# Performance work log

Measured on AMD Instinct MI355X. Metric: run time of the kernel, lower is better.

## Reference

```python
import jax, jax.numpy as jnp
import numpy as np

B, S, D, H = 2, 2048, 1024, 16
DK = D // H  # 64


def setup_inputs() -> dict:
    key = jax.random.key(0)
    ks = jax.random.split(key, 5)
    query_input = jax.random.normal(ks[0], (B, S, D), dtype=jnp.float32)
    # additive mask: 1.0 where attention is disallowed (causal upper triangle)
    mask = jnp.triu(jnp.ones((S, S), dtype=jnp.float32), k=1)[None, None, :, :]
    scale = 1.0 / np.sqrt(D)
    wq = jax.random.normal(ks[1], (D, D), dtype=jnp.float32) * scale
    wk = jax.random.normal(ks[2], (D, D), dtype=jnp.float32) * scale
    wv = jax.random.normal(ks[3], (D, D), dtype=jnp.float32) * scale
    wo = jax.random.normal(ks[4], (D, D), dtype=jnp.float32) * scale
    return {"query_input": query_input, "mask": mask, "wq": wq, "wk": wk, "wv": wv, "wo": wo}


def _split_heads(x):
    # [B, S, D] -> [B, H, S, DK]
    b, s, _ = x.shape
    return x.reshape(b, s, H, DK).transpose(0, 2, 1, 3)


def reference(query_input, mask, wq, wk, wv, wo):
    # self-attention: key_input = value_input = query_input
    q = _split_heads(query_input @ wq)  # [B, H, S, DK]
    k = _split_heads(query_input @ wk)
    v = _split_heads(query_input @ wv)
    scores = jnp.einsum('bhqd,bhkd->bhqk', q, k) / jnp.sqrt(jnp.float32(DK))
    scores = scores + mask * (-1e9)
    attn = jax.nn.softmax(scores, axis=-1)
    out = jnp.einsum('bhqk,bhkd->bhqd', attn, v)  # [B, H, S, DK]
    out = out.transpose(0, 2, 1, 3).reshape(query_input.shape[0], -1, D)
    return out @ wo
```

## Files before the change

kernel.cpp:

```cpp
#include <hip/hip_runtime.h>

typedef __attribute__((ext_vector_type(8))) short bf16x8;
typedef __attribute__((ext_vector_type(4))) float f32x4;
typedef __attribute__((ext_vector_type(4))) unsigned short u16x4;

#define S_LEN 2048
#define D_DIM 1024
#define NHEAD 16
#define DK 64
#define BH 32
#define MROWS 4096

__device__ __forceinline__ unsigned short f2bf(float f) {
    unsigned int u = __float_as_uint(f);
    u += 0x7fffu + ((u >> 16) & 1u);
    return (unsigned short)(u >> 16);
}

__device__ __forceinline__ unsigned int pk_bf16(float a, float b) {
    unsigned int r;
    asm("v_cvt_pk_bf16_f32 %0, %1, %2" : "=v"(r) : "v"(a), "v"(b));
    return r;
}

__device__ __forceinline__ float fexp2(float x) {
    return __builtin_amdgcn_exp2f(x);
}

__device__ __forceinline__ void gload16(const void* g, void* l) {
    __builtin_amdgcn_global_load_lds(
        (const __attribute__((address_space(1))) void*)g,
        (__attribute__((address_space(3))) void*)l, 16, 0, 0);
}

__global__ __launch_bounds__(256) void cast_x_kernel(const float* __restrict__ X,
                                                     unsigned short* __restrict__ Xb) {
    int idx = blockIdx.x * 256 + threadIdx.x;
    float4 v = ((const float4*)X)[idx];
    u16x4 o;
    o.x = f2bf(v.x); o.y = f2bf(v.y); o.z = f2bf(v.z); o.w = f2bf(v.w);
    ((u16x4*)Xb)[idx] = o;
}

__global__ __launch_bounds__(256) void wtrans_kernel(const float* __restrict__ wq,
                                                     const float* __restrict__ wk,
                                                     const float* __restrict__ wv,
                                                     const float* __restrict__ wo,
                                                     unsigned short* __restrict__ Wt) {
    int z = blockIdx.z;
    const float* W = (z == 0) ? wq : (z == 1) ? wk : (z == 2) ? wv : wo;
    unsigned short* O = Wt + (size_t)z * D_DIM * D_DIM;
    __shared__ float t[32][33];
    int tx = threadIdx.x, ty = threadIdx.y;
    int bx = blockIdx.x * 32;
    int by = blockIdx.y * 32;
#pragma unroll
    for (int i = 0; i < 4; ++i)
        t[ty + i * 8][tx] = W[(size_t)(by + ty + i * 8) * D_DIM + bx + tx];
    __syncthreads();
#pragma unroll
    for (int i = 0; i < 4; ++i)
        O[(size_t)(bx + ty + i * 8) * D_DIM + by + tx] = f2bf(t[tx][ty + i * 8]);
}

__device__ __forceinline__ void gemm_mainloop(const unsigned short* __restrict__ A,
                                              const unsigned short* __restrict__ Bt,
                                              int K, int m0, int n0,
                                              unsigned short* As, unsigned short* Bs,
                                              f32x4 acc[4][4]) {
    const int tid = threadIdx.x;
    const int lane = tid & 63, wid = tid >> 6;
    const int wr = wid >> 1, wc = wid & 1;
    const int fr = lane & 15, fk = (lane >> 4) * 8;
    for (int k0 = 0; k0 < K; k0 += 32) {
        __syncthreads();
#pragma unroll
        for (int c = 0; c < 2; ++c) {
            int idx = c * 256 + tid;
            int row = idx >> 2;
            int col = (idx & 3) * 8;
            int base = (c * 256 + wid * 64) * 8;
            gload16(&A[(size_t)(m0 + row) * K + k0 + col], &As[base]);
            gload16(&Bt[(size_t)(n0 + row) * K + k0 + col], &Bs[base]);
        }
        __syncthreads();
        bf16x8 af[4], bfr[4];
#pragma unroll
        for (int i = 0; i < 4; ++i)
            af[i] = *(const bf16x8*)&As[(wr * 64 + i * 16 + fr) * 32 + fk];
#pragma unroll
        for (int j = 0; j < 4; ++j)
            bfr[j] = *(const bf16x8*)&Bs[(wc * 64 + j * 16 + fr) * 32 + fk];
#pragma unroll
        for (int i = 0; i < 4; ++i)
#pragma unroll
            for (int j = 0; j < 4; ++j)
                acc[i][j] = __builtin_amdgcn_mfma_f32_16x16x32_bf16(af[i], bfr[j], acc[i][j], 0, 0, 0);
    }
}

#define QSCALE 0.18033688011112042f
__global__ __launch_bounds__(256) void gemm_qkv_kernel(const unsigned short* __restrict__ Xb,
                                                       const unsigned short* __restrict__ Wt,
                                                       unsigned short* __restrict__ QKV) {
    __shared__ __align__(16) unsigned short As[128 * 32];
    __shared__ __align__(16) unsigned short Bs[128 * 32];
    const unsigned short* Bt = Wt + (size_t)blockIdx.z * D_DIM * D_DIM;
    unsigned short* Out = QKV + (size_t)blockIdx.z * MROWS * D_DIM;
    int m0 = blockIdx.y * 128, n0 = blockIdx.x * 128;
    f32x4 acc[4][4] = {};
    gemm_mainloop(Xb, Bt, D_DIM, m0, n0, As, Bs, acc);
    const float qs = (blockIdx.z == 0) ? QSCALE : 1.0f;
    const int lane = threadIdx.x & 63, wid = threadIdx.x >> 6;
    const int wr = wid >> 1, wc = wid & 1;
#pragma unroll
    for (int i = 0; i < 4; ++i)
#pragma unroll
        for (int j = 0; j < 4; ++j)
#pragma unroll
            for (int r = 0; r < 4; ++r) {
                int gm = m0 + wr * 64 + i * 16 + (lane >> 4) * 4 + r;
                int gn = n0 + wc * 64 + j * 16 + (lane & 15);
                Out[(size_t)gm * D_DIM + gn] = f2bf(acc[i][j][r] * qs);
            }
}

__global__ __launch_bounds__(256) void vtrans_kernel(const unsigned short* __restrict__ V,
                                                     unsigned short* __restrict__ Vt) {
    __shared__ unsigned short tile[64][65];
    int bh = blockIdx.y;
    int b = bh >> 4, h = bh & 15;
    int s0 = blockIdx.x * 64;
    int t = threadIdx.x;
#pragma unroll
    for (int i = 0; i < 16; ++i) {
        int idx = i * 256 + t;
        int row = idx >> 6, col = idx & 63;
        tile[row][col] = V[((size_t)(b * S_LEN) + s0 + row) * D_DIM + h * DK + col];
    }
    __syncthreads();
#pragma unroll
    for (int i = 0; i < 16; ++i) {
        int idx = i * 256 + t;
        int dr = idx >> 6, sc = idx & 63;
        Vt[((size_t)bh * DK + dr) * S_LEN + s0 + sc] = tile[sc][dr];
    }
}

__global__ __launch_bounds__(512, 4) void attn_kernel(const unsigned short* __restrict__ QKV,
                                                      const unsigned short* __restrict__ Vt,
                                                      unsigned short* __restrict__ AO) {
    const int bh = blockIdx.x;
    const int y = blockIdx.y;
    const int qi = (y < 8) ? (15 - y) : (y - 8);
    const int tid = threadIdx.x, lane = tid & 63, wid = tid >> 6;
    const int fr = lane & 15, fkg = lane >> 4, fk = fkg * 8;
    const unsigned short* Q = QKV;
    const unsigned short* Kd = QKV + (size_t)MROWS * D_DIM;

    __shared__ __align__(16) unsigned short Ks[128][64];
    __shared__ __align__(16) unsigned short Vs[64][128];
    __shared__ __align__(16) unsigned short Ps[8][16][64];

    const int b = bh >> 4, h = bh & 15;
    const int rsw  = fr & 7;
    const int off0 = (fkg ^ rsw) * 8;
    const int off1 = ((4 + fkg) ^ rsw) * 8;

    const int i0 = tid, i1 = 512 + tid;
    const int kr0 = i0 >> 3, kc0 = ((i0 & 7) ^ (kr0 & 7)) * 8;
    const int kr1 = i1 >> 3, kc1 = ((i1 & 7) ^ (kr1 & 7)) * 8;
    const int vr0 = i0 >> 4, vc0 = ((i0 & 15) ^ (vr0 & 15)) * 8;
    const int vr1 = i1 >> 4, vc1 = ((i1 & 15) ^ (vr1 & 15)) * 8;
    const int sb0 = (wid * 64) * 8;
    const int sb1 = (512 + wid * 64) * 8;

    const int q0 = qi * 128;
    const int qr = q0 + wid * 16;

    bf16x8 qf0 = *(const bf16x8*)&Q[((size_t)(b * S_LEN) + qr + fr) * D_DIM + h * DK + fk];
    bf16x8 qf1 = *(const bf16x8*)&Q[((size_t)(b * S_LEN) + qr + fr) * D_DIM + h * DK + 32 + fk];

    f32x4 o[4] = {};
    float m = -1e30f, l = 0.f;
    const int ntiles = qi + 1;

    const unsigned short* kb = Kd + (size_t)(b * S_LEN) * D_DIM + h * DK;
    const unsigned short* vb = Vt + (size_t)bh * DK * S_LEN;

    gload16(kb + (size_t)kr0 * D_DIM + kc0, &Ks[0][0] + sb0);
    gload16(kb + (size_t)kr1 * D_DIM + kc1, &Ks[0][0] + sb1);
    gload16(vb + (size_t)vr0 * S_LEN + vc0, &Vs[0][0] + sb0);
    gload16(vb + (size_t)vr1 * S_LEN + vc1, &Vs[0][0] + sb1);

    for (int t = 0; t < ntiles; ++t) {
        __syncthreads();

        f32x4 s4[8];
        __builtin_amdgcn_s_setprio(1);
#pragma unroll
        for (int nj = 0; nj < 8; ++nj) {
            const unsigned short* krow = &Ks[nj * 16 + fr][0];
            bf16x8 kf0 = *(const bf16x8*)&krow[off0];
            bf16x8 kf1 = *(const bf16x8*)&krow[off1];
            f32x4 z = {};
            z = __builtin_amdgcn_mfma_f32_16x16x32_bf16(kf0, qf0, z, 0, 0, 0);
            z = __builtin_amdgcn_mfma_f32_16x16x32_bf16(kf1, qf1, z, 0, 0, 0);
            s4[nj] = z;
        }
        __builtin_amdgcn_s_setprio(0);

        if (t == ntiles - 1) {
            const int qoff = wid * 16 + fr;
#pragma unroll
            for (int nj = 0; nj < 8; ++nj)
#pragma unroll
                for (int r = 0; r < 4; ++r)
                    s4[nj][r] = (nj * 16 + fkg * 4 + r > qoff) ? -1e30f : s4[nj][r];
        }

        float mg[8];
#pragma unroll
        for (int nj = 0; nj < 8; ++nj)
            mg[nj] = fmaxf(fmaxf(s4[nj][0], s4[nj][1]), fmaxf(s4[nj][2], s4[nj][3]));
        float mt = fmaxf(fmaxf(fmaxf(mg[0], mg[1]), fmaxf(mg[2], mg[3])),
                         fmaxf(fmaxf(mg[4], mg[5]), fmaxf(mg[6], mg[7])));
        mt = fmaxf(mt, __shfl_xor(mt, 16, 64));
        mt = fmaxf(mt, __shfl_xor(mt, 32, 64));
        if (!__all(mt <= m + 8.0f)) {
            float mn = fmaxf(m, mt);
            float corr = fexp2(m - mn);
            m = mn;
            l *= corr;
            o[0] *= corr; o[1] *= corr; o[2] *= corr; o[3] *= corr;
        }
        float ps = 0.f;
        unsigned int pw[8][2];
#pragma unroll
        for (int nj = 0; nj < 8; ++nj) {
            float p0 = fexp2(s4[nj][0] - m);
            float p1 = fexp2(s4[nj][1] - m);
            float p2 = fexp2(s4[nj][2] - m);
            float p3 = fexp2(s4[nj][3] - m);
            ps += (p0 + p1) + (p2 + p3);
            pw[nj][0] = pk_bf16(p0, p1);
            pw[nj][1] = pk_bf16(p2, p3);
        }
        ps += __shfl_xor(ps, 16, 64);
        ps += __shfl_xor(ps, 32, 64);
        l += ps;

#pragma unroll
        for (int hf = 0; hf < 2; ++hf) {
#pragma unroll
            for (int nj = 0; nj < 4; ++nj) {
                int chunk = nj * 2 + (fkg >> 1);
                int el = (fkg & 1) * 4;
                *(uint2*)&Ps[wid][fr][((chunk ^ rsw) << 3) + el] =
                    make_uint2(pw[hf * 4 + nj][0], pw[hf * 4 + nj][1]);
            }
            bf16x8 pf0 = *(const bf16x8*)&Ps[wid][fr][off0];
            bf16x8 pf1 = *(const bf16x8*)&Ps[wid][fr][off1];
            __builtin_amdgcn_s_setprio(1);
#pragma unroll
            for (int j = 0; j < 4; ++j) {
                const unsigned short* vrow = &Vs[j * 16 + fr][0];
                bf16x8 vf0 = *(const bf16x8*)&vrow[((hf * 8 + fkg) ^ fr) * 8];
                bf16x8 vf1 = *(const bf16x8*)&vrow[((hf * 8 + 4 + fkg) ^ fr) * 8];
                o[j] = __builtin_amdgcn_mfma_f32_16x16x32_bf16(vf0, pf0, o[j], 0, 0, 0);
                o[j] = __builtin_amdgcn_mfma_f32_16x16x32_bf16(vf1, pf1, o[j], 0, 0, 0);
            }
            __builtin_amdgcn_s_setprio(0);
        }

        __syncthreads();
        if (t + 1 < ntiles) {
            const int kt = (t + 1) * 128;
            gload16(kb + (size_t)(kt + kr0) * D_DIM + kc0, &Ks[0][0] + sb0);
            gload16(kb + (size_t)(kt + kr1) * D_DIM + kc1, &Ks[0][0] + sb1);
            gload16(vb + (size_t)vr0 * S_LEN + kt + vc0, &Vs[0][0] + sb0);
            gload16(vb + (size_t)vr1 * S_LEN + kt + vc1, &Vs[0][0] + sb1);
        }
    }

    float inv = 1.0f / l;
    size_t rowoff = ((size_t)(b * S_LEN) + qr + fr) * D_DIM + h * DK;
#pragma unroll
    for (int j = 0; j < 4; ++j) {
        u16x4 w;
        w.x = f2bf(o[j][0] * inv); w.y = f2bf(o[j][1] * inv);
        w.z = f2bf(o[j][2] * inv); w.w = f2bf(o[j][3] * inv);
        *(u16x4*)&AO[rowoff + j * 16 + fkg * 4] = w;
    }
}

__global__ __launch_bounds__(256) void gemm_out_kernel(const unsigned short* __restrict__ AO,
                                                       const unsigned short* __restrict__ Wot,
                                                       float* __restrict__ out) {
    __shared__ __align__(16) unsigned short As[128 * 32];
    __shared__ __align__(16) unsigned short Bs[128 * 32];
    int m0 = blockIdx.y * 128, n0 = blockIdx.x * 128;
    f32x4 acc[4][4] = {};
    gemm_mainloop(AO, Wot, D_DIM, m0, n0, As, Bs, acc);
    const int lane = threadIdx.x & 63, wid = threadIdx.x >> 6;
    const int wr = wid >> 1, wc = wid & 1;
#pragma unroll
    for (int i = 0; i < 4; ++i)
#pragma unroll
        for (int j = 0; j < 4; ++j)
#pragma unroll
            for (int r = 0; r < 4; ++r) {
                int gm = m0 + wr * 64 + i * 16 + (lane >> 4) * 4 + r;
                int gn = n0 + wc * 64 + j * 16 + (lane & 15);
                out[(size_t)gm * D_DIM + gn] = acc[i][j][r];
            }
}

extern "C" void kernel_launch(void* const* d_in, const int* in_sizes, int n_in,
                              void* d_out, int out_size, void* d_ws, size_t ws_size,
                              hipStream_t stream) {
    (void)in_sizes; (void)n_in; (void)out_size; (void)ws_size;
    const float* X  = (const float*)d_in[0];
    const float* wq = (const float*)d_in[2];
    const float* wk = (const float*)d_in[3];
    const float* wv = (const float*)d_in[4];
    const float* wo = (const float*)d_in[5];

    char* ws = (char*)d_ws;
    unsigned short* Xb  = (unsigned short*)(ws);
    unsigned short* Wt  = (unsigned short*)(ws + ((size_t)8  << 20));
    unsigned short* QKV = (unsigned short*)(ws + ((size_t)16 << 20));
    unsigned short* Vt  = (unsigned short*)(ws + ((size_t)40 << 20));
    unsigned short* AO  = (unsigned short*)(ws + ((size_t)48 << 20));
    float* out = (float*)d_out;

    cast_x_kernel<<<4096, 256, 0, stream>>>(X, Xb);
    wtrans_kernel<<<dim3(32, 32, 4), dim3(32, 8), 0, stream>>>(wq, wk, wv, wo, Wt);
    gemm_qkv_kernel<<<dim3(8, 32, 3), 256, 0, stream>>>(Xb, Wt, QKV);
    vtrans_kernel<<<dim3(32, 32), 256, 0, stream>>>(QKV + (size_t)2 * MROWS * D_DIM, Vt);
    attn_kernel<<<dim3(32, 16), 512, 0, stream>>>(QKV, Vt, AO);
    gemm_out_kernel<<<dim3(8, 32), 256, 0, stream>>>(AO, Wt + (size_t)3 * D_DIM * D_DIM, out);
}
```

Before: 112.6 us.

## Pair light and heavy 64-row query tiles per attention block for causal balance

```diff
diff --git a/kernel.cpp b/kernel.cpp
--- a/kernel.cpp
+++ b/kernel.cpp
@@ -147,12 +147,11 @@
     }
 }
 
-__global__ __launch_bounds__(512, 4) void attn_kernel(const unsigned short* __restrict__ QKV,
+__global__ __launch_bounds__(256, 2) void attn_kernel(const unsigned short* __restrict__ QKV,
                                                       const unsigned short* __restrict__ Vt,
                                                       unsigned short* __restrict__ AO) {
     const int bh = blockIdx.x;
-    const int y = blockIdx.y;
-    const int qi = (y < 8) ? (15 - y) : (y - 8);
+    const int pair = blockIdx.y;
     const int tid = threadIdx.x, lane = tid & 63, wid = tid >> 6;
     const int fr = lane & 15, fkg = lane >> 4, fk = fkg * 8;
     const unsigned short* Q = QKV;
@@ -160,137 +159,144 @@
 
     __shared__ __align__(16) unsigned short Ks[128][64];
     __shared__ __align__(16) unsigned short Vs[64][128];
-    __shared__ __align__(16) unsigned short Ps[8][16][64];
+    __shared__ __align__(16) unsigned short Ps[4][16][64];
 
     const int b = bh >> 4, h = bh & 15;
     const int rsw  = fr & 7;
     const int off0 = (fkg ^ rsw) * 8;
     const int off1 = ((4 + fkg) ^ rsw) * 8;
 
-    const int i0 = tid, i1 = 512 + tid;
-    const int kr0 = i0 >> 3, kc0 = ((i0 & 7) ^ (kr0 & 7)) * 8;
-    const int kr1 = i1 >> 3, kc1 = ((i1 & 7) ^ (kr1 & 7)) * 8;
-    const int vr0 = i0 >> 4, vc0 = ((i0 & 15) ^ (vr0 & 15)) * 8;
-    const int vr1 = i1 >> 4, vc1 = ((i1 & 15) ^ (vr1 & 15)) * 8;
-    const int sb0 = (wid * 64) * 8;
-    const int sb1 = (512 + wid * 64) * 8;
-
-    const int q0 = qi * 128;
-    const int qr = q0 + wid * 16;
-
-    bf16x8 qf0 = *(const bf16x8*)&Q[((size_t)(b * S_LEN) + qr + fr) * D_DIM + h * DK + fk];
-    bf16x8 qf1 = *(const bf16x8*)&Q[((size_t)(b * S_LEN) + qr + fr) * D_DIM + h * DK + 32 + fk];
-
-    f32x4 o[4] = {};
-    float m = -1e30f, l = 0.f;
-    const int ntiles = qi + 1;
+    int kr[4], kc[4], vr[4], vc[4], sb[4];
+#pragma unroll
+    for (int c = 0; c < 4; ++c) {
+        int i = c * 256 + tid;
+        kr[c] = i >> 3;  kc[c] = ((i & 7) ^ (kr[c] & 7)) * 8;
+        vr[c] = i >> 4;  vc[c] = ((i & 15) ^ (vr[c] & 15)) * 8;
+        sb[c] = (c * 256 + wid * 64) * 8;
+    }
 
     const unsigned short* kb = Kd + (size_t)(b * S_LEN) * D_DIM + h * DK;
     const unsigned short* vb = Vt + (size_t)bh * DK * S_LEN;
 
-    gload16(kb + (size_t)kr0 * D_DIM + kc0, &Ks[0][0] + sb0);
-    gload16(kb + (size_t)kr1 * D_DIM + kc1, &Ks[0][0] + sb1);
-    gload16(vb + (size_t)vr0 * S_LEN + vc0, &Vs[0][0] + sb0);
-    gload16(vb + (size_t)vr1 * S_LEN + vc1, &Vs[0][0] + sb1);
-
-    for (int t = 0; t < ntiles; ++t) {
-        __syncthreads();
-
-        f32x4 s4[8];
-        __builtin_amdgcn_s_setprio(1);
-#pragma unroll
-        for (int nj = 0; nj < 8; ++nj) {
-            const unsigned short* krow = &Ks[nj * 16 + fr][0];
-            bf16x8 kf0 = *(const bf16x8*)&krow[off0];
-            bf16x8 kf1 = *(const bf16x8*)&krow[off1];
-            f32x4 z = {};
-            z = __builtin_amdgcn_mfma_f32_16x16x32_bf16(kf0, qf0, z, 0, 0, 0);
-            z = __builtin_amdgcn_mfma_f32_16x16x32_bf16(kf1, qf1, z, 0, 0, 0);
-            s4[nj] = z;
+#pragma unroll
+    for (int pass = 0; pass < 2; ++pass) {
+        const int qi = pass ? (31 - pair) : pair;
+        const int q0 = qi * 64;
+        const int qr = q0 + wid * 16;
+        const int ntiles = (qi >> 1) + 1;
+
+        bf16x8 qf0 = *(const bf16x8*)&Q[((size_t)(b * S_LEN) + qr + fr) * D_DIM + h * DK + fk];
+        bf16x8 qf1 = *(const bf16x8*)&Q[((size_t)(b * S_LEN) + qr + fr) * D_DIM + h * DK + 32 + fk];
+
+        f32x4 o[4] = {};
+        float m = -1e30f, l = 0.f;
+
+#pragma unroll
+        for (int c = 0; c < 4; ++c) {
+            gload16(kb + (size_t)kr[c] * D_DIM + kc[c], &Ks[0][0] + sb[c]);
+            gload16(vb + (size_t)vr[c] * S_LEN + vc[c], &Vs[0][0] + sb[c]);
         }
-        __builtin_amdgcn_s_setprio(0);
-
-        if (t == ntiles - 1) {
-            const int qoff = wid * 16 + fr;
+
+        for (int t = 0; t < ntiles; ++t) {
+            __syncthreads();
+
+            f32x4 s4[8];
+            __builtin_amdgcn_s_setprio(1);
+#pragma unroll
+            for (int nj = 0; nj < 8; ++nj) {
+                const unsigned short* krow = &Ks[nj * 16 + fr][0];
+                bf16x8 kf0 = *(const bf16x8*)&krow[off0];
+                bf16x8 kf1 = *(const bf16x8*)&krow[off1];
+                f32x4 z = {};
+                z = __builtin_amdgcn_mfma_f32_16x16x32_bf16(kf0, qf0, z, 0, 0, 0);
+                z = __builtin_amdgcn_mfma_f32_16x16x32_bf16(kf1, qf1, z, 0, 0, 0);
+                s4[nj] = z;
+            }
+            __builtin_amdgcn_s_setprio(0);
+
+            if (t == ntiles - 1) {
+                const int qoff = qr + fr - (ntiles - 1) * 128;
+#pragma unroll
+                for (int nj = 0; nj < 8; ++nj)
+#pragma unroll
+                    for (int r = 0; r < 4; ++r)
+                        s4[nj][r] = (nj * 16 + fkg * 4 + r > qoff) ? -1e30f : s4[nj][r];
+            }
+
+            float mg[8];
 #pragma unroll
             for (int nj = 0; nj < 8; ++nj)
-#pragma unroll
-                for (int r = 0; r < 4; ++r)
-                    s4[nj][r] = (nj * 16 + fkg * 4 + r > qoff) ? -1e30f : s4[nj][r];
+                mg[nj] = fmaxf(fmaxf(s4[nj][0], s4[nj][1]), fmaxf(s4[nj][2], s4[nj][3]));
+            float mt = fmaxf(fmaxf(fmaxf(mg[0], mg[1]), fmaxf(mg[2], mg[3])),
+                             fmaxf(fmaxf(mg[4], mg[5]), fmaxf(mg[6], mg[7])));
+            mt = fmaxf(mt, __shfl_xor(mt, 16, 64));
+            mt = fmaxf(mt, __shfl_xor(mt, 32, 64));
+            if (!__all(mt <= m + 8.0f)) {
+                float mn = fmaxf(m, mt);
+                float corr = fexp2(m - mn);
+                m = mn;
+                l *= corr;
+                o[0] *= corr; o[1] *= corr; o[2] *= corr; o[3] *= corr;
+            }
+            float ps = 0.f;
+            unsigned int pw[8][2];
+#pragma unroll
+            for (int nj = 0; nj < 8; ++nj) {
+                float p0 = fexp2(s4[nj][0] - m);
+                float p1 = fexp2(s4[nj][1] - m);
+                float p2 = fexp2(s4[nj][2] - m);
+                float p3 = fexp2(s4[nj][3] - m);
+                ps += (p0 + p1) + (p2 + p3);
+                pw[nj][0] = pk_bf16(p0, p1);
+                pw[nj][1] = pk_bf16(p2, p3);
+            }
+            ps += __shfl_xor(ps, 16, 64);
+            ps += __shfl_xor(ps, 32, 64);
+            l += ps;
+
+#pragma unroll
+            for (int hf = 0; hf < 2; ++hf) {
+#pragma unroll
+                for (int nj = 0; nj < 4; ++nj) {
+                    int chunk = nj * 2 + (fkg >> 1);
+                    int el = (fkg & 1) * 4;
+                    *(uint2*)&Ps[wid][fr][((chunk ^ rsw) << 3) + el] =
+                        make_uint2(pw[hf * 4 + nj][0], pw[hf * 4 + nj][1]);
+                }
+                bf16x8 pf0 = *(const bf16x8*)&Ps[wid][fr][off0];
+                bf16x8 pf1 = *(const bf16x8*)&Ps[wid][fr][off1];
+                __builtin_amdgcn_s_setprio(1);
+#pragma unroll
+                for (int j = 0; j < 4; ++j) {
+                    const unsigned short* vrow = &Vs[j * 16 + fr][0];
+                    bf16x8 vf0 = *(const bf16x8*)&vrow[((hf * 8 + fkg) ^ fr) * 8];
+                    bf16x8 vf1 = *(const bf16x8*)&vrow[((hf * 8 + 4 + fkg) ^ fr) * 8];
+                    o[j] = __builtin_amdgcn_mfma_f32_16x16x32_bf16(vf0, pf0, o[j], 0, 0, 0);
+                    o[j] = __builtin_amdgcn_mfma_f32_16x16x32_bf16(vf1, pf1, o[j], 0, 0, 0);
+                }
+                __builtin_amdgcn_s_setprio(0);
+            }
+
+            __syncthreads();
+            if (t + 1 < ntiles) {
+                const int kt = (t + 1) * 128;
+#pragma unroll
+                for (int c = 0; c < 4; ++c) {
+                    gload16(kb + (size_t)(kt + kr[c]) * D_DIM + kc[c], &Ks[0][0] + sb[c]);
+                    gload16(vb + (size_t)vr[c] * S_LEN + kt + vc[c], &Vs[0][0] + sb[c]);
+                }
+            }
         }
 
-        float mg[8];
-#pragma unroll
-        for (int nj = 0; nj < 8; ++nj)
-            mg[nj] = fmaxf(fmaxf(s4[nj][0], s4[nj][1]), fmaxf(s4[nj][2], s4[nj][3]));
-        float mt = fmaxf(fmaxf(fmaxf(mg[0], mg[1]), fmaxf(mg[2], mg[3])),
-                         fmaxf(fmaxf(mg[4], mg[5]), fmaxf(mg[6], mg[7])));
-        mt = fmaxf(mt, __shfl_xor(mt, 16, 64));
-        mt = fmaxf(mt, __shfl_xor(mt, 32, 64));
-        if (!__all(mt <= m + 8.0f)) {
-            float mn = fmaxf(m, mt);
-            float corr = fexp2(m - mn);
-            m = mn;
-            l *= corr;
-            o[0] *= corr; o[1] *= corr; o[2] *= corr; o[3] *= corr;
+        float inv = 1.0f / l;
+        size_t rowoff = ((size_t)(b * S_LEN) + qr + fr) * D_DIM + h * DK;
+#pragma unroll
+        for (int j = 0; j < 4; ++j) {
+            u16x4 w;
+            w.x = f2bf(o[j][0] * inv); w.y = f2bf(o[j][1] * inv);
+            w.z = f2bf(o[j][2] * inv); w.w = f2bf(o[j][3] * inv);
+            *(u16x4*)&AO[rowoff + j * 16 + fkg * 4] = w;
         }
-        float ps = 0.f;
-        unsigned int pw[8][2];
-#pragma unroll
-        for (int nj = 0; nj < 8; ++nj) {
-            float p0 = fexp2(s4[nj][0] - m);
-            float p1 = fexp2(s4[nj][1] - m);
-            float p2 = fexp2(s4[nj][2] - m);
-            float p3 = fexp2(s4[nj][3] - m);
-            ps += (p0 + p1) + (p2 + p3);
-            pw[nj][0] = pk_bf16(p0, p1);
-            pw[nj][1] = pk_bf16(p2, p3);
-        }
-        ps += __shfl_xor(ps, 16, 64);
-        ps += __shfl_xor(ps, 32, 64);
-        l += ps;
-
-#pragma unroll
-        for (int hf = 0; hf < 2; ++hf) {
-#pragma unroll
-            for (int nj = 0; nj < 4; ++nj) {
-                int chunk = nj * 2 + (fkg >> 1);
-                int el = (fkg & 1) * 4;
-                *(uint2*)&Ps[wid][fr][((chunk ^ rsw) << 3) + el] =
-                    make_uint2(pw[hf * 4 + nj][0], pw[hf * 4 + nj][1]);
-            }
-            bf16x8 pf0 = *(const bf16x8*)&Ps[wid][fr][off0];
-            bf16x8 pf1 = *(const bf16x8*)&Ps[wid][fr][off1];
-            __builtin_amdgcn_s_setprio(1);
-#pragma unroll
-            for (int j = 0; j < 4; ++j) {
-                const unsigned short* vrow = &Vs[j * 16 + fr][0];
-                bf16x8 vf0 = *(const bf16x8*)&vrow[((hf * 8 + fkg) ^ fr) * 8];
-                bf16x8 vf1 = *(const bf16x8*)&vrow[((hf * 8 + 4 + fkg) ^ fr) * 8];
-                o[j] = __builtin_amdgcn_mfma_f32_16x16x32_bf16(vf0, pf0, o[j], 0, 0, 0);
-                o[j] = __builtin_amdgcn_mfma_f32_16x16x32_bf16(vf1, pf1, o[j], 0, 0, 0);
-            }
-            __builtin_amdgcn_s_setprio(0);
-        }
-
-        __syncthreads();
-        if (t + 1 < ntiles) {
-            const int kt = (t + 1) * 128;
-            gload16(kb + (size_t)(kt + kr0) * D_DIM + kc0, &Ks[0][0] + sb0);
-            gload16(kb + (size_t)(kt + kr1) * D_DIM + kc1, &Ks[0][0] + sb1);
-            gload16(vb + (size_t)vr0 * S_LEN + kt + vc0, &Vs[0][0] + sb0);
-            gload16(vb + (size_t)vr1 * S_LEN + kt + vc1, &Vs[0][0] + sb1);
-        }
-    }
-
-    float inv = 1.0f / l;
-    size_t rowoff = ((size_t)(b * S_LEN) + qr + fr) * D_DIM + h * DK;
-#pragma unroll
-    for (int j = 0; j < 4; ++j) {
-        u16x4 w;
-        w.x = f2bf(o[j][0] * inv); w.y = f2bf(o[j][1] * inv);
-        w.z = f2bf(o[j][2] * inv); w.w = f2bf(o[j][3] * inv);
-        *(u16x4*)&AO[rowoff + j * 16 + fkg * 4] = w;
     }
 }
 
@@ -338,6 +344,6 @@
     wtrans_kernel<<<dim3(32, 32, 4), dim3(32, 8), 0, stream>>>(wq, wk, wv, wo, Wt);
     gemm_qkv_kernel<<<dim3(8, 32, 3), 256, 0, stream>>>(Xb, Wt, QKV);
     vtrans_kernel<<<dim3(32, 32), 256, 0, stream>>>(QKV + (size_t)2 * MROWS * D_DIM, Vt);
-    attn_kernel<<<dim3(32, 16), 512, 0, stream>>>(QKV, Vt, AO);
+    attn_kernel<<<dim3(32, 16), 256, 0, stream>>>(QKV, Vt, AO);
     gemm_out_kernel<<<dim3(8, 32), 256, 0, stream>>>(AO, Wt + (size_t)3 * D_DIM * D_DIM, out);
 }
```

Result: slower. 115.7 us (+2.7%).

## Double-buffer GEMM LDS tiles and fuse V transpose into QKV epilogue

Applied to the files above, without the earlier changes.

```diff
diff --git a/kernel.cpp b/kernel.cpp
--- a/kernel.cpp
+++ b/kernel.cpp
@@ -72,78 +72,91 @@
     const int lane = tid & 63, wid = tid >> 6;
     const int wr = wid >> 1, wc = wid & 1;
     const int fr = lane & 15, fk = (lane >> 4) * 8;
-    for (int k0 = 0; k0 < K; k0 += 32) {
-        __syncthreads();
-#pragma unroll
-        for (int c = 0; c < 2; ++c) {
-            int idx = c * 256 + tid;
-            int row = idx >> 2;
-            int col = (idx & 3) * 8;
-            int base = (c * 256 + wid * 64) * 8;
-            gload16(&A[(size_t)(m0 + row) * K + k0 + col], &As[base]);
-            gload16(&Bt[(size_t)(n0 + row) * K + k0 + col], &Bs[base]);
-        }
-        __syncthreads();
+    const int nt = K >> 5;
+#pragma unroll
+    for (int c = 0; c < 2; ++c) {
+        int idx = c * 256 + tid;
+        int row = idx >> 2;
+        int col = (idx & 3) * 8;
+        int base = (c * 256 + wid * 64) * 8;
+        gload16(&A[(size_t)(m0 + row) * K + col], &As[base]);
+        gload16(&Bt[(size_t)(n0 + row) * K + col], &Bs[base]);
+    }
+    __syncthreads();
+    int buf = 0;
+    for (int t = 0; t < nt; ++t) {
+        if (t + 1 < nt) {
+            int k0 = (t + 1) * 32;
+#pragma unroll
+            for (int c = 0; c < 2; ++c) {
+                int idx = c * 256 + tid;
+                int row = idx >> 2;
+                int col = (idx & 3) * 8;
+                int base = ((buf ^ 1) * 512 + c * 256 + wid * 64) * 8;
+                gload16(&A[(size_t)(m0 + row) * K + k0 + col], &As[base]);
+                gload16(&Bt[(size_t)(n0 + row) * K + k0 + col], &Bs[base]);
+            }
+        }
+        const unsigned short* Ab = As + buf * 512 * 8;
+        const unsigned short* Bb = Bs + buf * 512 * 8;
         bf16x8 af[4], bfr[4];
 #pragma unroll
         for (int i = 0; i < 4; ++i)
-            af[i] = *(const bf16x8*)&As[(wr * 64 + i * 16 + fr) * 32 + fk];
+            af[i] = *(const bf16x8*)&Ab[(wr * 64 + i * 16 + fr) * 32 + fk];
 #pragma unroll
         for (int j = 0; j < 4; ++j)
-            bfr[j] = *(const bf16x8*)&Bs[(wc * 64 + j * 16 + fr) * 32 + fk];
+            bfr[j] = *(const bf16x8*)&Bb[(wc * 64 + j * 16 + fr) * 32 + fk];
 #pragma unroll
         for (int i = 0; i < 4; ++i)
 #pragma unroll
             for (int j = 0; j < 4; ++j)
                 acc[i][j] = __builtin_amdgcn_mfma_f32_16x16x32_bf16(af[i], bfr[j], acc[i][j], 0, 0, 0);
+        __syncthreads();
+        buf ^= 1;
     }
 }
 
 #define QSCALE 0.18033688011112042f
 __global__ __launch_bounds__(256) void gemm_qkv_kernel(const unsigned short* __restrict__ Xb,
                                                        const unsigned short* __restrict__ Wt,
-                                                       unsigned short* __restrict__ QKV) {
-    __shared__ __align__(16) unsigned short As[128 * 32];
-    __shared__ __align__(16) unsigned short Bs[128 * 32];
+                                                       unsigned short* __restrict__ QKV,
+                                                       unsigned short* __restrict__ Vtp) {
+    __shared__ __align__(16) unsigned short As[2 * 128 * 32];
+    __shared__ __align__(16) unsigned short Bs[2 * 128 * 32];
     const unsigned short* Bt = Wt + (size_t)blockIdx.z * D_DIM * D_DIM;
-    unsigned short* Out = QKV + (size_t)blockIdx.z * MROWS * D_DIM;
     int m0 = blockIdx.y * 128, n0 = blockIdx.x * 128;
     f32x4 acc[4][4] = {};
     gemm_mainloop(Xb, Bt, D_DIM, m0, n0, As, Bs, acc);
-    const float qs = (blockIdx.z == 0) ? QSCALE : 1.0f;
     const int lane = threadIdx.x & 63, wid = threadIdx.x >> 6;
     const int wr = wid >> 1, wc = wid & 1;
-#pragma unroll
-    for (int i = 0; i < 4; ++i)
-#pragma unroll
-        for (int j = 0; j < 4; ++j)
-#pragma unroll
-            for (int r = 0; r < 4; ++r) {
-                int gm = m0 + wr * 64 + i * 16 + (lane >> 4) * 4 + r;
+    if (blockIdx.z == 2) {
+        const int b = m0 >> 11;
+#pragma unroll
+        for (int i = 0; i < 4; ++i)
+#pragma unroll
+            for (int j = 0; j < 4; ++j) {
+                int gm = m0 + wr * 64 + i * 16 + (lane >> 4) * 4;
                 int gn = n0 + wc * 64 + j * 16 + (lane & 15);
-                Out[(size_t)gm * D_DIM + gn] = f2bf(acc[i][j][r] * qs);
-            }
-}
-
-__global__ __launch_bounds__(256) void vtrans_kernel(const unsigned short* __restrict__ V,
-                                                     unsigned short* __restrict__ Vt) {
-    __shared__ unsigned short tile[64][65];
-    int bh = blockIdx.y;
-    int b = bh >> 4, h = bh & 15;
-    int s0 = blockIdx.x * 64;
-    int t = threadIdx.x;
-#pragma unroll
-    for (int i = 0; i < 16; ++i) {
-        int idx = i * 256 + t;
-        int row = idx >> 6, col = idx & 63;
-        tile[row][col] = V[((size_t)(b * S_LEN) + s0 + row) * D_DIM + h * DK + col];
-    }
-    __syncthreads();
-#pragma unroll
-    for (int i = 0; i < 16; ++i) {
-        int idx = i * 256 + t;
-        int dr = idx >> 6, sc = idx & 63;
-        Vt[((size_t)bh * DK + dr) * S_LEN + s0 + sc] = tile[sc][dr];
+                int bh = b * NHEAD + (gn >> 6);
+                int dk = gn & 63;
+                u16x4 w;
+                w.x = f2bf(acc[i][j][0]); w.y = f2bf(acc[i][j][1]);
+                w.z = f2bf(acc[i][j][2]); w.w = f2bf(acc[i][j][3]);
+                *(u16x4*)&Vtp[((size_t)bh * DK + dk) * S_LEN + (gm & 2047)] = w;
+            }
+    } else {
+        unsigned short* Out = QKV + (size_t)blockIdx.z * MROWS * D_DIM;
+        const float qs = (blockIdx.z == 0) ? QSCALE : 1.0f;
+#pragma unroll
+        for (int i = 0; i < 4; ++i)
+#pragma unroll
+            for (int j = 0; j < 4; ++j)
+#pragma unroll
+                for (int r = 0; r < 4; ++r) {
+                    int gm = m0 + wr * 64 + i * 16 + (lane >> 4) * 4 + r;
+                    int gn = n0 + wc * 64 + j * 16 + (lane & 15);
+                    Out[(size_t)gm * D_DIM + gn] = f2bf(acc[i][j][r] * qs);
+                }
     }
 }
 
@@ -297,8 +310,8 @@
 __global__ __launch_bounds__(256) void gemm_out_kernel(const unsigned short* __restrict__ AO,
                                                        const unsigned short* __restrict__ Wot,
                                                        float* __restrict__ out) {
-    __shared__ __align__(16) unsigned short As[128 * 32];
-    __shared__ __align__(16) unsigned short Bs[128 * 32];
+    __shared__ __align__(16) unsigned short As[2 * 128 * 32];
+    __shared__ __align__(16) unsigned short Bs[2 * 128 * 32];
     int m0 = blockIdx.y * 128, n0 = blockIdx.x * 128;
     f32x4 acc[4][4] = {};
     gemm_mainloop(AO, Wot, D_DIM, m0, n0, As, Bs, acc);
@@ -336,8 +349,7 @@
 
     cast_x_kernel<<<4096, 256, 0, stream>>>(X, Xb);
     wtrans_kernel<<<dim3(32, 32, 4), dim3(32, 8), 0, stream>>>(wq, wk, wv, wo, Wt);
-    gemm_qkv_kernel<<<dim3(8, 32, 3), 256, 0, stream>>>(Xb, Wt, QKV);
-    vtrans_kernel<<<dim3(32, 32), 256, 0, stream>>>(QKV + (size_t)2 * MROWS * D_DIM, Vt);
+    gemm_qkv_kernel<<<dim3(8, 32, 3), 256, 0, stream>>>(Xb, Wt, QKV, Vt);
     attn_kernel<<<dim3(32, 16), 512, 0, stream>>>(QKV, Vt, AO);
     gemm_out_kernel<<<dim3(8, 32), 256, 0, stream>>>(AO, Wt + (size_t)3 * D_DIM * D_DIM, out);
 }
```

New measurement: 117.3 us, median of 3. 4.1% more time.

## Read K and V fragments directly from global memory instead of LDS staging

Applied to the files above, without the earlier changes.

```diff
diff --git a/kernel.cpp b/kernel.cpp
--- a/kernel.cpp
+++ b/kernel.cpp
@@ -158,8 +158,6 @@
     const unsigned short* Q = QKV;
     const unsigned short* Kd = QKV + (size_t)MROWS * D_DIM;
 
-    __shared__ __align__(16) unsigned short Ks[128][64];
-    __shared__ __align__(16) unsigned short Vs[64][128];
     __shared__ __align__(16) unsigned short Ps[8][16][64];
 
     const int b = bh >> 4, h = bh & 15;
@@ -167,14 +165,6 @@
     const int off0 = (fkg ^ rsw) * 8;
     const int off1 = ((4 + fkg) ^ rsw) * 8;
 
-    const int i0 = tid, i1 = 512 + tid;
-    const int kr0 = i0 >> 3, kc0 = ((i0 & 7) ^ (kr0 & 7)) * 8;
-    const int kr1 = i1 >> 3, kc1 = ((i1 & 7) ^ (kr1 & 7)) * 8;
-    const int vr0 = i0 >> 4, vc0 = ((i0 & 15) ^ (vr0 & 15)) * 8;
-    const int vr1 = i1 >> 4, vc1 = ((i1 & 15) ^ (vr1 & 15)) * 8;
-    const int sb0 = (wid * 64) * 8;
-    const int sb1 = (512 + wid * 64) * 8;
-
     const int q0 = qi * 128;
     const int qr = q0 + wid * 16;
 
@@ -188,21 +178,16 @@
     const unsigned short* kb = Kd + (size_t)(b * S_LEN) * D_DIM + h * DK;
     const unsigned short* vb = Vt + (size_t)bh * DK * S_LEN;
 
-    gload16(kb + (size_t)kr0 * D_DIM + kc0, &Ks[0][0] + sb0);
-    gload16(kb + (size_t)kr1 * D_DIM + kc1, &Ks[0][0] + sb1);
-    gload16(vb + (size_t)vr0 * S_LEN + vc0, &Vs[0][0] + sb0);
-    gload16(vb + (size_t)vr1 * S_LEN + vc1, &Vs[0][0] + sb1);
-
     for (int t = 0; t < ntiles; ++t) {
-        __syncthreads();
+        const int kt = t * 128;
 
         f32x4 s4[8];
         __builtin_amdgcn_s_setprio(1);
 #pragma unroll
         for (int nj = 0; nj < 8; ++nj) {
-            const unsigned short* krow = &Ks[nj * 16 + fr][0];
-            bf16x8 kf0 = *(const bf16x8*)&krow[off0];
-            bf16x8 kf1 = *(const bf16x8*)&krow[off1];
+            const unsigned short* krow = &kb[(size_t)(kt + nj * 16 + fr) * D_DIM];
+            bf16x8 kf0 = *(const bf16x8*)&krow[fk];
+            bf16x8 kf1 = *(const bf16x8*)&krow[32 + fk];
             f32x4 z = {};
             z = __builtin_amdgcn_mfma_f32_16x16x32_bf16(kf0, qf0, z, 0, 0, 0);
             z = __builtin_amdgcn_mfma_f32_16x16x32_bf16(kf1, qf1, z, 0, 0, 0);
@@ -264,22 +249,13 @@
             __builtin_amdgcn_s_setprio(1);
 #pragma unroll
             for (int j = 0; j < 4; ++j) {
-                const unsigned short* vrow = &Vs[j * 16 + fr][0];
-                bf16x8 vf0 = *(const bf16x8*)&vrow[((hf * 8 + fkg) ^ fr) * 8];
-                bf16x8 vf1 = *(const bf16x8*)&vrow[((hf * 8 + 4 + fkg) ^ fr) * 8];
+                const unsigned short* vrow = &vb[(size_t)(j * 16 + fr) * S_LEN + kt];
+                bf16x8 vf0 = *(const bf16x8*)&vrow[(hf * 8 + fkg) * 8];
+                bf16x8 vf1 = *(const bf16x8*)&vrow[(hf * 8 + 4 + fkg) * 8];
                 o[j] = __builtin_amdgcn_mfma_f32_16x16x32_bf16(vf0, pf0, o[j], 0, 0, 0);
                 o[j] = __builtin_amdgcn_mfma_f32_16x16x32_bf16(vf1, pf1, o[j], 0, 0, 0);
             }
             __builtin_amdgcn_s_setprio(0);
-        }
-
-        __syncthreads();
-        if (t + 1 < ntiles) {
-            const int kt = (t + 1) * 128;
-            gload16(kb + (size_t)(kt + kr0) * D_DIM + kc0, &Ks[0][0] + sb0);
-            gload16(kb + (size_t)(kt + kr1) * D_DIM + kc1, &Ks[0][0] + sb1);
-            gload16(vb + (size_t)vr0 * S_LEN + kt + vc0, &Vs[0][0] + sb0);
-            gload16(vb + (size_t)vr1 * S_LEN + kt + vc1, &Vs[0][0] + sb1);
         }
     }
 
```

Result: slower. 198.6 us (+76.4%).
